# Optimization experiments

Hardware: AMD Instinct MI355X
Metric: run time of the kernel (lower is better)

The kernel has to match this reference:

```python
import jax, jax.numpy as jnp
import numpy as np

T, B, C, H, W, L, K = 8, 8, 64, 96, 96, 2, 3


def _conv(x, w):
    # x: [B,C,H,W], w: [O,I,K,K], SAME padding, stride 1
    return jax.lax.conv_general_dilated(
        x, w, window_strides=(1, 1), padding='SAME',
        dimension_numbers=('NCHW', 'OIHW', 'NCHW'))


def setup_inputs() -> dict:
    key = jax.random.key(0)
    ks = jax.random.split(key, 17)
    wscale = 0.04  # ~ 1/sqrt(64*9) fan-in
    out = {'x': jax.random.normal(ks[0], (T, B, C, H, W), jnp.float32)}
    wnames = ['wxi', 'whi', 'wci', 'wxf', 'whf', 'wcf', 'wxc', 'whc',
              'wxo', 'who', 'wco']
    for i, n in enumerate(wnames):
        out[n] = jax.random.normal(ks[1 + i], (L, C, C, K, K), jnp.float32) * wscale
    bnames = ['b_i', 'b_f', 'b_c', 'b_o']
    for i, n in enumerate(bnames):
        out[n] = jax.random.normal(ks[12 + i], (L, C), jnp.float32) * 0.01
    return out


def reference(x, wxi, whi, wci, wxf, whf, wcf, wxc, whc, wxo, who, wco,
              b_i, b_f, b_c, b_o):
    # x: [T,B,C,H,W]. Peephole Conv-LSTM; note original module's quirk:
    # output gate uses w_hc (with its bias) applied to the NEW cell state.
    hs = cs = None
    for l in range(L):
        Wxi, Whi, Wci = wxi[l], whi[l], wci[l]
        Wxf, Whf, Wcf = wxf[l], whf[l], wcf[l]
        Wxc, Whc = wxc[l], whc[l]
        Wxo, Who, Wco = wxo[l], who[l], wco[l]
        bi = b_i[l][None, :, None, None]
        bf = b_f[l][None, :, None, None]
        bc = b_c[l][None, :, None, None]
        bo = b_o[l][None, :, None, None]

        def step(carry, xt, Wxi=Wxi, Whi=Whi, Wci=Wci, Wxf=Wxf, Whf=Whf,
                 Wcf=Wcf, Wxc=Wxc, Whc=Whc, Wxo=Wxo, Who=Who,
                 bi=bi, bf=bf, bc=bc, bo=bo):
            h, c = carry
            i = jax.nn.sigmoid(_conv(xt, Wxi) + _conv(h, Whi) + bi + _conv(c, Wci))
            f = jax.nn.sigmoid(_conv(xt, Wxf) + _conv(h, Whf) + bf + _conv(c, Wcf))
            c_t = jnp.tanh(_conv(xt, Wxc) + _conv(h, Whc) + bc)
            c_new = c_t * i + c * f
            # faithful to source: w_hc (with its bias) on the new cell state
            o = jax.nn.sigmoid(_conv(xt, Wxo) + _conv(h, Who) + bo
                               + _conv(c_new, Whc) + bc)
            h_new = o * jnp.tanh(c_new)
            return (h_new, c_new), (h_new, c_new)

        h0 = jnp.zeros((x.shape[1], C, H, W), x.dtype)
        c0 = jnp.zeros((x.shape[1], C, H, W), x.dtype)
        _, (hs, cs) = jax.lax.scan(step, (h0, c0), x)
        x = hs  # next layer consumes this layer's hidden sequence
    return hs, cs  # each [T,B,C,H,W]
```

## Files before the change

kernel.cpp:

```cpp
#include <hip/hip_runtime.h>
#include <math.h>

#define TT 8
#define BB 8
#define CC 64
#define HH 96
#define WW 96
#define LL 2
#define HW   (HH * WW)
#define CHW  (CC * HW)
#define BCHW (BB * CHW)
#define TBCHW (TT * BCHW)
#define WSZ  (CC * CC * 9)

typedef _Float16 f16;
typedef __attribute__((ext_vector_type(8))) _Float16 f16x8;
typedef __attribute__((ext_vector_type(4))) _Float16 f16x4;
typedef __attribute__((ext_vector_type(4))) float f32x4;

__device__ __forceinline__ float sigmoidf_(float x) {
    return 1.0f / (1.0f + __expf(-x));
}
__device__ __forceinline__ float tanhf_(float x) {
    float e = __expf(2.f * x);
    return 1.f - 2.f / (e + 1.f);
}


#define SLOT_B   9834496ull
#define PLANE_B  1229312ull
#define SLOT_F   (SLOT_B / 2)
#define GPLANE_F 4718592ull
#define WT_F     36864
#define XHALF_F  18816
#define WHALF_F  18432

struct WPtrs { const float* p[10]; };

__device__ __forceinline__ void gl_lds16(const void* g, void* lds_base) {
    __builtin_amdgcn_global_load_lds(
        (const __attribute__((address_space(1))) unsigned int*)g,
        (__attribute__((address_space(3))) unsigned int*)lds_base, 16, 0, 0);
}

__global__ __launch_bounds__(256) void wprep(WPtrs wsrcs, f16* Wf) {
    const int tap = blockIdx.x, ti = blockIdx.y, l = blockIdx.z;
    const float* src = wsrcs.p[ti] + l * WSZ;
    f16* dst = Wf + (size_t)(l * 10 + ti) * WT_F;
    for (int r = 0; r < 16; ++r) {
        int lin = r * 256 + threadIdx.x;
        int co = lin >> 6, ci = lin & 63;
        float v = src[(co * 64 + ci) * 9 + tap];
        int half = ci >> 5, e = ci & 31, s = e >> 3;
        int p = (s ^ co) & 3;
        dst[((half * 9 + tap) * 64 + co) * 32 + p * 8 + (e & 7)] = (f16)v;
    }
}

__global__ __launch_bounds__(256) void bzero(char* slots) {
    unsigned u = blockIdx.x * 256 + threadIdx.x;
    if (u >= 248320u) return;
    unsigned plane = u / 3104u;
    unsigned r = u % 3104u;
    unsigned i = r >> 3, c = r & 7;
    int y, x;
    if (i < 98)       { y = 0;           x = i; }
    else if (i < 196) { y = 97;          x = i - 98; }
    else if (i < 292) { y = i - 196 + 1; x = 0; }
    else              { y = i - 292 + 1; x = 97; }
    uint4 z = make_uint4(0, 0, 0, 0);
    *(uint4*)(slots + (size_t)plane * PLANE_B + (size_t)(y * 98 + x) * 128 + c * 16) = z;
}

__global__ __launch_bounds__(256) void xprep(const float* __restrict__ x, f16* slots) {
    const int t = blockIdx.y;
    const int b = blockIdx.x / 96, y = blockIdx.x % 96;
    f16* slot = slots + (size_t)t * SLOT_F;
    for (int r = 0; r < 3; ++r) {
        int u = r * 256 + threadIdx.x;
        int px = u >> 3, c = u & 7;
        int half = c >> 2, p = c & 3;
        int sc = (p ^ (px + 1)) & 3;
        int ci0 = half * 32 + sc * 8;
        const float* sp = x + ((((size_t)t * BB + b) * CC + ci0) * HH + y) * WW + px;
        union { f16 h[8]; uint4 q; } pk;
#pragma unroll
        for (int j = 0; j < 8; ++j) pk.h[j] = (f16)sp[(size_t)j * HW];
        f16* dp = slot + ((size_t)b * 9604 + (y + 1) * 98 + (px + 1)) * 64 + half * 32 + p * 8;
        *(uint4*)dp = pk.q;
    }
}

__device__ __forceinline__ void stage_phase(const char* __restrict__ xb_h, int y0,
                                            const char* __restrict__ wsec_h,
                                            int w, int lane, f16* Xs, f16* Wl) {
    const char* xc = xb_h + (size_t)y0 * 12544;
    const int cb = w * 588;
#pragma unroll
    for (int i = 0; i < 9; ++i) {
        const int c = cb + i * 64 + lane;
        gl_lds16(xc + (size_t)(c >> 2) * 128 + (c & 3) * 16,
                 (char*)Xs + (size_t)(cb + i * 64) * 16);
    }
    if (lane < 12) {
        const int c = cb + 576 + lane;
        gl_lds16(xc + (size_t)(c >> 2) * 128 + (c & 3) * 16,
                 (char*)Xs + (size_t)(cb + 576) * 16);
    }
    const int cw = w * 576;
#pragma unroll
    for (int i = 0; i < 9; ++i) {
        gl_lds16(wsec_h + (size_t)(cw + i * 64 + lane) * 16,
                 (char*)Wl + (size_t)(cw + i * 64) * 16);
    }
}

__device__ __forceinline__ void mfma_phase(const f16* Xs, const f16* Wl,
                                           int w, int aBase, int d0, int d1, int d2,
                                           f32x4 acc[4][6]) {
#pragma unroll
    for (int tap = 0; tap < 9; ++tap) {
        const int dy = tap / 3, dx = tap % 3;
        const f16* Ar = &Wl[tap * 2048 + aBase];
        f16x8 a0 = *(const f16x8*)(Ar);
        f16x8 a1 = *(const f16x8*)(Ar + 512);
        f16x8 a2 = *(const f16x8*)(Ar + 1024);
        f16x8 a3 = *(const f16x8*)(Ar + 1536);
        const int doff = (dx == 0) ? d0 : (dx == 1) ? d1 : d2;
        const f16* Br = &Xs[(w + dy) * 3136 + doff];
#pragma unroll
        for (int nt = 0; nt < 6; ++nt) {
            f16x8 bf = *(const f16x8*)(Br + nt * 512);
            acc[0][nt] = __builtin_amdgcn_mfma_f32_16x16x32_f16(a0, bf, acc[0][nt], 0, 0, 0);
            acc[1][nt] = __builtin_amdgcn_mfma_f32_16x16x32_f16(a1, bf, acc[1][nt], 0, 0, 0);
            acc[2][nt] = __builtin_amdgcn_mfma_f32_16x16x32_f16(a2, bf, acc[2][nt], 0, 0, 0);
            acc[3][nt] = __builtin_amdgcn_mfma_f32_16x16x32_f16(a3, bf, acc[3][nt], 0, 0, 0);
        }
    }
}

struct GArgsN {
    const f16* in[3];
    const f16* w[4][3];
    f16* G;
    int nsecA, nsecB;
};

__global__ __launch_bounds__(256, 1) void gates_n(GArgsN A) {
    __shared__ __align__(16) f16 Xs[2 * XHALF_F];
    __shared__ __align__(16) f16 Wl[2 * WHALF_F];
    const int bid = blockIdx.x;
    const int b = bid & 7, rr = bid >> 3, g = rr & 3, y0 = (rr >> 2) * 4;
    const int tid = threadIdx.x, w = tid >> 6, lane = tid & 63;
    const int pxl = lane & 15, kg = lane >> 4;

    const int aBase = pxl * 32 + (((kg ^ pxl) & 3) << 3);
    const int d0 = (pxl + 0) * 32 + (((kg ^ (pxl + 0)) & 3) << 3);
    const int d1 = (pxl + 1) * 32 + (((kg ^ (pxl + 1)) & 3) << 3);
    const int d2 = (pxl + 2) * 32 + (((kg ^ (pxl + 2)) & 3) << 3);

    f32x4 acc[4][6];
#pragma unroll
    for (int mt = 0; mt < 4; ++mt)
#pragma unroll
        for (int nt = 0; nt < 6; ++nt) acc[mt][nt] = (f32x4){0.f, 0.f, 0.f, 0.f};

    const char* xb0 = (const char*)(A.in[0] + (size_t)b * 614656);
    const char* xb1 = (const char*)(A.in[1] + (size_t)b * 614656);
    const char* xb2 = (const char*)(A.in[2] + (size_t)b * 614656);
    const char* wp0 = (const char*)A.w[g][0];
    const char* wp1 = (const char*)A.w[g][1];
    const char* wp2 = (const char*)A.w[g][2];
    const int NP = 2 * ((g < 2) ? A.nsecA : A.nsecB);

    stage_phase(xb0, y0, wp0, w, lane, Xs, Wl);
    __syncthreads();
    for (int p = 0; p < NP; ++p) {
        const int cur = p & 1;
        if (p + 1 < NP) {
            const int s1 = (p + 1) >> 1, h1 = (p + 1) & 1;
            const char* xb_s = (s1 == 0) ? xb0 : (s1 == 1) ? xb1 : xb2;
            const char* wp_s = (s1 == 0) ? wp0 : (s1 == 1) ? wp1 : wp2;
            stage_phase(xb_s + h1 * 64, y0, wp_s + h1 * 36864, w, lane,
                        Xs + (cur ^ 1) * XHALF_F, Wl + (cur ^ 1) * WHALF_F);
        }
        mfma_phase(Xs + cur * XHALF_F, Wl + cur * WHALF_F,
                   w, aBase, d0, d1, d2, acc);
        __syncthreads();
    }

    f16* Gg = A.G + (size_t)g * GPLANE_F + ((size_t)b * 9216 + (y0 + w) * 96) * 64;
#pragma unroll
    for (int mt = 0; mt < 4; ++mt)
#pragma unroll
        for (int nt = 0; nt < 6; ++nt) {
            union { f16 h[4]; uint2 q; } pk;
#pragma unroll
            for (int r = 0; r < 4; ++r) pk.h[r] = (f16)acc[mt][nt][r];
            *(uint2*)(Gg + (size_t)(nt * 16 + pxl) * 64 + mt * 16 + kg * 4) = pk.q;
        }
}

__global__ __launch_bounds__(256) void pointwise_n(const f16* __restrict__ G,
                                                   const f16* __restrict__ cprev,
                                                   const float* __restrict__ bi,
                                                   const float* __restrict__ bf,
                                                   const float* __restrict__ bc,
                                                   f16* __restrict__ cnew,
                                                   float* __restrict__ cs_out) {
    const int b = blockIdx.y;
    const int u = blockIdx.x * 256 + threadIdx.x;
    const int pix = u >> 3, o = u & 7;
    const int ci0 = o * 8;
    const f16x8 gi = *(const f16x8*)(G + ((size_t)b * 9216 + pix) * 64 + ci0);
    const f16x8 gf = *(const f16x8*)(G + GPLANE_F + ((size_t)b * 9216 + pix) * 64 + ci0);
    const f16x8 gc = *(const f16x8*)(G + 2 * GPLANE_F + ((size_t)b * 9216 + pix) * 64 + ci0);
    const int py = pix / 96 + 1, pxp = pix % 96 + 1;
    const size_t pad_off = ((size_t)b * 9604 + py * 98 + pxp) * 64;
    const int half = o >> 2, p = ((o & 3) ^ pxp) & 3;
    const size_t sw_off = pad_off + half * 32 + p * 8;
    f16x8 cp = (f16x8)(_Float16)0.f;
    if (cprev) cp = *(const f16x8*)(cprev + sw_off);
    union { f16 h[8]; uint4 q; } outp;
    float cv[8];
#pragma unroll
    for (int j = 0; j < 8; ++j) {
        float vbi = bi[ci0 + j], vbf = bf[ci0 + j], vbc = bc[ci0 + j];
        float c = tanhf_((float)gc[j] + vbc) * sigmoidf_((float)gi[j] + vbi)
                + (float)cp[j] * sigmoidf_((float)gf[j] + vbf);
        cv[j] = c;
        outp.h[j] = (f16)c;
    }
    *(uint4*)(cnew + sw_off) = outp.q;
    if (cs_out) {
        float* op = cs_out + (size_t)b * CHW + (size_t)ci0 * HW + pix;
#pragma unroll
        for (int j = 0; j < 8; ++j) op[(size_t)j * HW] = cv[j];
    }
}

__global__ __launch_bounds__(256, 1) void out_n(const f16* __restrict__ cnew,
                                                const f16* __restrict__ whc,
                                                const f16* __restrict__ Go,
                                                const float* __restrict__ bo,
                                                const float* __restrict__ bc,
                                                f16* __restrict__ hslot,
                                                float* __restrict__ hs_out) {
    __shared__ __align__(16) f16 Xs[2 * XHALF_F];
    __shared__ __align__(16) f16 Wl[2 * WHALF_F];
    const int bid = blockIdx.x;
    const int b = bid & 7, y0 = (bid >> 3) * 4;
    const int tid = threadIdx.x, w = tid >> 6, lane = tid & 63;
    const int pxl = lane & 15, kg = lane >> 4;

    const int aBase = pxl * 32 + (((kg ^ pxl) & 3) << 3);
    const int d0 = (pxl + 0) * 32 + (((kg ^ (pxl + 0)) & 3) << 3);
    const int d1 = (pxl + 1) * 32 + (((kg ^ (pxl + 1)) & 3) << 3);
    const int d2 = (pxl + 2) * 32 + (((kg ^ (pxl + 2)) & 3) << 3);

    f32x4 acc[4][6];
#pragma unroll
    for (int mt = 0; mt < 4; ++mt)
#pragma unroll
        for (int nt = 0; nt < 6; ++nt) acc[mt][nt] = (f32x4){0.f, 0.f, 0.f, 0.f};

    const char* xb = (const char*)(cnew + (size_t)b * 614656);
    stage_phase(xb, y0, (const char*)whc, w, lane, Xs, Wl);
    __syncthreads();
    for (int p = 0; p < 2; ++p) {
        const int cur = p & 1;
        if (p == 0)
            stage_phase(xb + 64, y0, (const char*)whc + 36864, w, lane,
                        Xs + XHALF_F, Wl + WHALF_F);
        mfma_phase(Xs + cur * XHALF_F, Wl + cur * WHALF_F,
                   w, aBase, d0, d1, d2, acc);
        __syncthreads();
    }

    const int y = y0 + w;
#pragma unroll
    for (int mt = 0; mt < 4; ++mt) {
        const int cob = mt * 16 + kg * 4;
        float vb[4];
#pragma unroll
        for (int r = 0; r < 4; ++r) vb[r] = bo[cob + r] + bc[cob + r];
        const int half = mt >> 1;
        const int sq = (mt * 2 + (kg >> 1)) & 3;
        const int lo4 = (kg & 1) * 4;
#pragma unroll
        for (int nt = 0; nt < 6; ++nt) {
            const int px = nt * 16 + pxl;
            const int pix = y * 96 + px;
            const size_t pad_off = ((size_t)b * 9604 + (y + 1) * 98 + (px + 1)) * 64;
            const int p = (sq ^ (px + 1)) & 3;
            const size_t qoff = pad_off + half * 32 + p * 8 + lo4;
            f16x4 cq = *(const f16x4*)(cnew + qoff);
            f16x4 gq = *(const f16x4*)(Go + ((size_t)b * 9216 + pix) * 64 + cob);
            union { f16 h[4]; uint2 q; } hq;
            float hv[4];
#pragma unroll
            for (int r = 0; r < 4; ++r) {
                float opre = acc[mt][nt][r] + (float)gq[r] + vb[r];
                hv[r] = sigmoidf_(opre) * tanhf_((float)cq[r]);
                hq.h[r] = (f16)hv[r];
            }
            *(uint2*)(hslot + qoff) = hq.q;
            if (hs_out) {
                float* op = hs_out + (size_t)b * CHW + (size_t)cob * HW + pix;
#pragma unroll
                for (int r = 0; r < 4; ++r) op[(size_t)r * HW] = hv[r];
            }
        }
    }
}


#define XROW 3136
#define XSZ  (6 * XROW)
#define WROW 2048
#define WSZL (9 * WROW)

__device__ __forceinline__ void conv_section(
    const float* __restrict__ inb, const float* __restrict__ wp,
    int y0, int tid, f16* Xs, f16* Wl,
    int w, int aBase, int d0, int d1, int d2, f32x4 acc[4][6])
{
    for (int ci0 = 0; ci0 < 64; ci0 += 32) {
        __syncthreads();
        for (int i = tid; i < 9408; i += 256) {
            int x = i % 98; int r = i / 98; int yy = r % 6; int c2 = r / 6;
            int gy = y0 - 1 + yy, gx = x - 1;
            float v0 = 0.f, v1 = 0.f;
            if ((unsigned)gy < 96u && (unsigned)gx < 96u) {
                const float* p = inb + (size_t)(ci0 + 2 * c2) * HW + gy * WW + gx;
                v0 = p[0]; v1 = p[HW];
            }
            union { f16 h[2]; unsigned u; } pk;
            pk.h[0] = (f16)v0; pk.h[1] = (f16)v1;
            int e = 2 * c2;
            int idx = (yy * 98 + x) * 32 + ((((e >> 3) ^ x) & 3) << 3) + (e & 7);
            *(unsigned*)&Xs[idx] = pk.u;
        }
        for (int i = tid; i < 9216; i += 256) {
            int c2 = i & 15; int co = (i >> 4) & 63; int tap = i >> 10;
            const float* p = wp + ((size_t)co * CC + ci0 + 2 * c2) * 9 + tap;
            union { f16 h[2]; unsigned u; } pk;
            pk.h[0] = (f16)p[0]; pk.h[1] = (f16)p[9];
            int e = 2 * c2;
            int idx = tap * WROW + co * 32 + ((((e >> 3) ^ co) & 3) << 3) + (e & 7);
            *(unsigned*)&Wl[idx] = pk.u;
        }
        __syncthreads();
        mfma_phase(Xs, Wl, w, aBase, d0, d1, d2, acc);
    }
}

struct GArgs {
    const float* in[3];
    const float* w[4][3];
    f16* G;
};

__global__ __launch_bounds__(256) void gates_mfma(GArgs A) {
    __shared__ __align__(16) f16 Xs[XSZ];
    __shared__ __align__(16) f16 Wl[WSZL];
    const int g = blockIdx.z, b = blockIdx.y, y0 = blockIdx.x * 4;
    const int tid = threadIdx.x;
    const int w = tid >> 6, lane = tid & 63;
    const int pxl = lane & 15, kg = lane >> 4;
    const int aBase = pxl * 32 + (((kg ^ pxl) & 3) << 3);
    const int d0 = (pxl + 0) * 32 + (((kg ^ (pxl + 0)) & 3) << 3);
    const int d1 = (pxl + 1) * 32 + (((kg ^ (pxl + 1)) & 3) << 3);
    const int d2 = (pxl + 2) * 32 + (((kg ^ (pxl + 2)) & 3) << 3);
    f32x4 acc[4][6];
#pragma unroll
    for (int mt = 0; mt < 4; ++mt)
#pragma unroll
        for (int nt = 0; nt < 6; ++nt) acc[mt][nt] = (f32x4){0.f, 0.f, 0.f, 0.f};
    for (int s = 0; s < 3; ++s) {
        const float* inp = A.in[s];
        const float* wp = A.w[g][s];
        if (!inp || !wp) continue;
        conv_section(inp + (size_t)b * CHW, wp, y0, tid, Xs, Wl, w, aBase, d0, d1, d2, acc);
    }
    f16* Gp = A.G + (size_t)(g * BB + b) * CHW;
    const int y = y0 + w;
#pragma unroll
    for (int mt = 0; mt < 4; ++mt)
#pragma unroll
        for (int r = 0; r < 4; ++r) {
            const int co = mt * 16 + kg * 4 + r;
            f16* rp = Gp + (size_t)co * HW + y * WW + pxl;
#pragma unroll
            for (int nt = 0; nt < 6; ++nt) rp[nt * 16] = (f16)acc[mt][nt][r];
        }
}

__global__ __launch_bounds__(256) void pointwise_c(const f16* __restrict__ G,
                                                   const float* __restrict__ cprev,
                                                   const float* __restrict__ bi,
                                                   const float* __restrict__ bf,
                                                   const float* __restrict__ bc,
                                                   float* __restrict__ cnew) {
    int flat = (blockIdx.x * 256 + threadIdx.x) * 4;
    if (flat >= BCHW) return;
    int co = (flat / HW) & 63;
    f16x4 gi = *(const f16x4*)(G + flat);
    f16x4 gf = *(const f16x4*)(G + (size_t)BCHW + flat);
    f16x4 gc = *(const f16x4*)(G + 2 * (size_t)BCHW + flat);
    float4 cp = make_float4(0.f, 0.f, 0.f, 0.f);
    if (cprev) cp = *(const float4*)(cprev + flat);
    float vbi = bi[co], vbf = bf[co], vbc = bc[co];
    float4 r;
    r.x = tanhf_((float)gc.x + vbc) * sigmoidf_((float)gi.x + vbi) + cp.x * sigmoidf_((float)gf.x + vbf);
    r.y = tanhf_((float)gc.y + vbc) * sigmoidf_((float)gi.y + vbi) + cp.y * sigmoidf_((float)gf.y + vbf);
    r.z = tanhf_((float)gc.z + vbc) * sigmoidf_((float)gi.z + vbi) + cp.z * sigmoidf_((float)gf.z + vbf);
    r.w = tanhf_((float)gc.w + vbc) * sigmoidf_((float)gi.w + vbi) + cp.w * sigmoidf_((float)gf.w + vbf);
    *(float4*)(cnew + flat) = r;
}

__global__ __launch_bounds__(256) void out_mfma(const float* __restrict__ cnew,
                                                const float* __restrict__ wp,
                                                const f16* __restrict__ Go,
                                                const float* __restrict__ bo,
                                                const float* __restrict__ bc,
                                                float* __restrict__ hout) {
    __shared__ __align__(16) f16 Xs[XSZ];
    __shared__ __align__(16) f16 Wl[WSZL];
    const int b = blockIdx.y, y0 = blockIdx.x * 4;
    const int tid = threadIdx.x;
    const int w = tid >> 6, lane = tid & 63;
    const int pxl = lane & 15, kg = lane >> 4;
    const int aBase = pxl * 32 + (((kg ^ pxl) & 3) << 3);
    const int d0 = (pxl + 0) * 32 + (((kg ^ (pxl + 0)) & 3) << 3);
    const int d1 = (pxl + 1) * 32 + (((kg ^ (pxl + 1)) & 3) << 3);
    const int d2 = (pxl + 2) * 32 + (((kg ^ (pxl + 2)) & 3) << 3);
    f32x4 acc[4][6];
#pragma unroll
    for (int mt = 0; mt < 4; ++mt)
#pragma unroll
        for (int nt = 0; nt < 6; ++nt) acc[mt][nt] = (f32x4){0.f, 0.f, 0.f, 0.f};
    const float* cb = cnew + (size_t)b * CHW;
    conv_section(cb, wp, y0, tid, Xs, Wl, w, aBase, d0, d1, d2, acc);
    const f16* Gb = Go + (size_t)b * CHW;
    float* hb = hout + (size_t)b * CHW;
    const int y = y0 + w;
#pragma unroll
    for (int mt = 0; mt < 4; ++mt)
#pragma unroll
        for (int r = 0; r < 4; ++r) {
            const int co = mt * 16 + kg * 4 + r;
            const float vbv = bo[co] + bc[co];
            const size_t off0 = (size_t)co * HW + y * WW + pxl;
#pragma unroll
            for (int nt = 0; nt < 6; ++nt) {
                size_t off = off0 + nt * 16;
                float opre = acc[mt][nt][r] + (float)Gb[off] + vbv;
                hb[off] = sigmoidf_(opre) * tanhf_(cb[off]);
            }
        }
}


extern "C" void kernel_launch(void* const* d_in, const int* in_sizes, int n_in,
                              void* d_out, int out_size, void* d_ws, size_t ws_size,
                              hipStream_t stream) {
    const float* x = (const float*)d_in[0];
    const float* w_[11];
    for (int i = 0; i < 11; ++i) w_[i] = (const float*)d_in[1 + i];
    const float* b_[4];
    for (int i = 0; i < 4; ++i) b_[i] = (const float*)d_in[12 + i];

    float* out = (float*)d_out;
    float* hs = out;
    float* cs = out + TBCHW;

    const size_t G_B = 4ull * GPLANE_F * 2ull;
    const size_t WF_B = 2ull * 10ull * WT_F * 2ull;
    const size_t NEED = 10ull * SLOT_B + G_B + WF_B;

    if (ws_size >= NEED) {
        char* ws = (char*)d_ws;
        f16* slots = (f16*)ws;
        f16* G = (f16*)(ws + 10ull * SLOT_B);
        f16* Wf = (f16*)(ws + 10ull * SLOT_B + G_B);

        WPtrs wps;
        for (int i = 0; i < 10; ++i) wps.p[i] = w_[i];

        wprep<<<dim3(9, 10, 2), 256, 0, stream>>>(wps, Wf);
        bzero<<<dim3(971), 256, 0, stream>>>((char*)slots);
        xprep<<<dim3(96 * BB, TT), 256, 0, stream>>>(x, slots);

        for (int l = 0; l < LL; ++l) {
            const f16* WT[10];
            for (int ti = 0; ti < 10; ++ti) WT[ti] = Wf + (size_t)(l * 10 + ti) * WT_F;
            const float* bi = b_[0] + l * CC;
            const float* bf = b_[1] + l * CC;
            const float* bc = b_[2] + l * CC;
            const float* bo = b_[3] + l * CC;

            for (int t = 0; t < TT; ++t) {
                f16* xt = slots + (size_t)t * SLOT_F;
                f16* hprev = (t == 0) ? nullptr : slots + (size_t)(t - 1) * SLOT_F;
                f16* cprev = (t == 0) ? nullptr
                                      : slots + (size_t)(8 + ((t - 1) & 1)) * SLOT_F;
                f16* cnew = slots + (size_t)(8 + (t & 1)) * SLOT_F;

                GArgsN a;
                if (t == 0) {
                    a.in[0] = xt; a.in[1] = xt; a.in[2] = xt;
                    a.w[0][0] = WT[0]; a.w[0][1] = WT[0]; a.w[0][2] = WT[0];
                    a.w[1][0] = WT[3]; a.w[1][1] = WT[3]; a.w[1][2] = WT[3];
                    a.w[2][0] = WT[6]; a.w[2][1] = WT[6]; a.w[2][2] = WT[6];
                    a.w[3][0] = WT[8]; a.w[3][1] = WT[8]; a.w[3][2] = WT[8];
                    a.nsecA = 1; a.nsecB = 1;
                } else {
                    a.in[0] = xt; a.in[1] = hprev; a.in[2] = cprev;
                    a.w[0][0] = WT[0]; a.w[0][1] = WT[1]; a.w[0][2] = WT[2];
                    a.w[1][0] = WT[3]; a.w[1][1] = WT[4]; a.w[1][2] = WT[5];
                    a.w[2][0] = WT[6]; a.w[2][1] = WT[7]; a.w[2][2] = WT[7];
                    a.w[3][0] = WT[8]; a.w[3][1] = WT[9]; a.w[3][2] = WT[9];
                    a.nsecA = 3; a.nsecB = 2;
                }
                a.G = G;
                gates_n<<<dim3(768), 256, 0, stream>>>(a);
                pointwise_n<<<dim3(288, BB), 256, 0, stream>>>(
                    G, cprev, bi, bf, bc, cnew,
                    (l == 1) ? (cs + (size_t)t * BCHW) : nullptr);
                out_n<<<dim3(192), 256, 0, stream>>>(
                    cnew, WT[7], G + 3 * GPLANE_F, bo, bc,
                    xt,
                    (l == 1) ? (hs + (size_t)t * BCHW) : nullptr);
            }
        }
        return;
    }

    f16* G = (f16*)d_ws;
    float* c0 = (float*)d_ws + 2 * (size_t)BCHW;
    float* c1 = c0 + BCHW;

    for (int l = 0; l < LL; ++l) {
        const float* wxi = w_[0] + l * WSZ;
        const float* whi = w_[1] + l * WSZ;
        const float* wci = w_[2] + l * WSZ;
        const float* wxf = w_[3] + l * WSZ;
        const float* whf = w_[4] + l * WSZ;
        const float* wcf = w_[5] + l * WSZ;
        const float* wxc = w_[6] + l * WSZ;
        const float* whc = w_[7] + l * WSZ;
        const float* wxo = w_[8] + l * WSZ;
        const float* who = w_[9] + l * WSZ;
        const float* bi = b_[0] + l * CC;
        const float* bf = b_[1] + l * CC;
        const float* bc = b_[2] + l * CC;
        const float* bo = b_[3] + l * CC;

        for (int t = 0; t < TT; ++t) {
            const float* xt = (l == 0) ? (x + (size_t)t * BCHW) : (hs + (size_t)t * BCHW);
            const float* hprev = (t == 0) ? nullptr : (hs + (size_t)(t - 1) * BCHW);
            const float* cprev = (t == 0) ? nullptr
                : (l == 0 ? (((t - 1) & 1) ? c1 : c0) : (cs + (size_t)(t - 1) * BCHW));
            float* cnew = (l == 0) ? ((t & 1) ? c1 : c0) : (cs + (size_t)t * BCHW);

            GArgs a;
            a.in[0] = xt; a.in[1] = hprev; a.in[2] = cprev;
            a.w[0][0] = wxi; a.w[0][1] = whi; a.w[0][2] = wci;
            a.w[1][0] = wxf; a.w[1][1] = whf; a.w[1][2] = wcf;
            a.w[2][0] = wxc; a.w[2][1] = whc; a.w[2][2] = nullptr;
            a.w[3][0] = wxo; a.w[3][1] = who; a.w[3][2] = nullptr;
            a.G = G;
            gates_mfma<<<dim3(24, BB, 4), 256, 0, stream>>>(a);
            pointwise_c<<<dim3(BCHW / 1024), 256, 0, stream>>>(G, cprev, bi, bf, bc, cnew);
            out_mfma<<<dim3(24, BB), 256, 0, stream>>>(cnew, whc, G + (size_t)3 * BCHW,
                                                       bo, bc, hs + (size_t)t * BCHW);
        }
    }
}
```

Baseline: 1.716 ms.

## Fuse cell-state pointwise kernel into output-gate conv kernel, computing c_new into LDS

Merges the pointwise cell-update kernel and the output-gate convolution kernel into one. Each block computes c_new for its rows plus a one-row halo directly into shared memory, then runs the w_hc convolution from LDS. This removes a launch and the global round trip of c_new before the conv. The cost is redundant computation of the halo rows, one block per CU, and fewer blocks (192) for the pointwise part. It also switches G loads/stores and the hs/cs float outputs to nontemporal accesses to reduce cache pollution.

```diff
diff --git a/kernel.cpp b/kernel.cpp
--- a/kernel.cpp
+++ b/kernel.cpp
@@ -24,6 +24,16 @@
 __device__ __forceinline__ float tanhf_(float x) {
     float e = __expf(2.f * x);
     return 1.f - 2.f / (e + 1.f);
+}
+
+__device__ __forceinline__ void nt_store_u2(void* p, uint2 v) {
+    __builtin_nontemporal_store(*(unsigned long long*)&v, (unsigned long long*)p);
+}
+__device__ __forceinline__ f16x8 nt_load8(const f16* p) {
+    return __builtin_nontemporal_load((const f16x8*)p);
+}
+__device__ __forceinline__ f16x4 nt_load4(const f16* p) {
+    return __builtin_nontemporal_load((const f16x4*)p);
 }
 
 
@@ -197,55 +207,20 @@
             union { f16 h[4]; uint2 q; } pk;
 #pragma unroll
             for (int r = 0; r < 4; ++r) pk.h[r] = (f16)acc[mt][nt][r];
-            *(uint2*)(Gg + (size_t)(nt * 16 + pxl) * 64 + mt * 16 + kg * 4) = pk.q;
-        }
-}
-
-__global__ __launch_bounds__(256) void pointwise_n(const f16* __restrict__ G,
-                                                   const f16* __restrict__ cprev,
-                                                   const float* __restrict__ bi,
-                                                   const float* __restrict__ bf,
-                                                   const float* __restrict__ bc,
-                                                   f16* __restrict__ cnew,
-                                                   float* __restrict__ cs_out) {
-    const int b = blockIdx.y;
-    const int u = blockIdx.x * 256 + threadIdx.x;
-    const int pix = u >> 3, o = u & 7;
-    const int ci0 = o * 8;
-    const f16x8 gi = *(const f16x8*)(G + ((size_t)b * 9216 + pix) * 64 + ci0);
-    const f16x8 gf = *(const f16x8*)(G + GPLANE_F + ((size_t)b * 9216 + pix) * 64 + ci0);
-    const f16x8 gc = *(const f16x8*)(G + 2 * GPLANE_F + ((size_t)b * 9216 + pix) * 64 + ci0);
-    const int py = pix / 96 + 1, pxp = pix % 96 + 1;
-    const size_t pad_off = ((size_t)b * 9604 + py * 98 + pxp) * 64;
-    const int half = o >> 2, p = ((o & 3) ^ pxp) & 3;
-    const size_t sw_off = pad_off + half * 32 + p * 8;
-    f16x8 cp = (f16x8)(_Float16)0.f;
-    if (cprev) cp = *(const f16x8*)(cprev + sw_off);
-    union { f16 h[8]; uint4 q; } outp;
-    float cv[8];
-#pragma unroll
-    for (int j = 0; j < 8; ++j) {
-        float vbi = bi[ci0 + j], vbf = bf[ci0 + j], vbc = bc[ci0 + j];
-        float c = tanhf_((float)gc[j] + vbc) * sigmoidf_((float)gi[j] + vbi)
-                + (float)cp[j] * sigmoidf_((float)gf[j] + vbf);
-        cv[j] = c;
-        outp.h[j] = (f16)c;
-    }
-    *(uint4*)(cnew + sw_off) = outp.q;
-    if (cs_out) {
-        float* op = cs_out + (size_t)b * CHW + (size_t)ci0 * HW + pix;
-#pragma unroll
-        for (int j = 0; j < 8; ++j) op[(size_t)j * HW] = cv[j];
-    }
-}
-
-__global__ __launch_bounds__(256, 1) void out_n(const f16* __restrict__ cnew,
-                                                const f16* __restrict__ whc,
-                                                const f16* __restrict__ Go,
-                                                const float* __restrict__ bo,
-                                                const float* __restrict__ bc,
-                                                f16* __restrict__ hslot,
-                                                float* __restrict__ hs_out) {
+            nt_store_u2(Gg + (size_t)(nt * 16 + pxl) * 64 + mt * 16 + kg * 4, pk.q);
+        }
+}
+
+__global__ __launch_bounds__(256, 1) void cellout_n(
+    const f16* __restrict__ G,
+    const f16* __restrict__ cprev,
+    const float* __restrict__ bi, const float* __restrict__ bf,
+    const float* __restrict__ bc, const float* __restrict__ bo,
+    const f16* __restrict__ whc,
+    f16* __restrict__ cnew,
+    f16* __restrict__ hslot,
+    float* __restrict__ cs_out,
+    float* __restrict__ hs_out) {
     __shared__ __align__(16) f16 Xs[2 * XHALF_F];
     __shared__ __align__(16) f16 Wl[2 * WHALF_F];
     const int bid = blockIdx.x;
@@ -253,6 +228,79 @@
     const int tid = threadIdx.x, w = tid >> 6, lane = tid & 63;
     const int pxl = lane & 15, kg = lane >> 4;
 
+    {
+        const char* wh = (const char*)whc;
+        const int cw = w * 576;
+#pragma unroll
+        for (int i = 0; i < 9; ++i) {
+            gl_lds16(wh + (size_t)(cw + i * 64 + lane) * 16,
+                     (char*)Wl + (size_t)(cw + i * 64) * 16);
+            gl_lds16(wh + 36864 + (size_t)(cw + i * 64 + lane) * 16,
+                     (char*)(Wl + WHALF_F) + (size_t)(cw + i * 64) * 16);
+        }
+    }
+
+    const int o = tid & 7;
+    const int ci0 = o * 8;
+    const int halfo = o >> 2;
+    float vbi[8], vbf[8], vbc[8];
+#pragma unroll
+    for (int j = 0; j < 8; ++j) { vbi[j] = bi[ci0 + j]; vbf[j] = bf[ci0 + j]; vbc[j] = bc[ci0 + j]; }
+
+    const size_t gb = (size_t)b * 9216;
+    for (int r6 = 0; r6 < 6; ++r6) {
+        const int gy = y0 - 1 + r6;
+        const bool inimg = (unsigned)gy < 96u;
+#pragma unroll
+        for (int j = 0; j < 3; ++j) {
+            const int px = j * 32 + (tid >> 3);
+            const int pxp = px + 1;
+            const int p = ((o & 3) ^ pxp) & 3;
+            union { f16 h[8]; uint4 q; } outp;
+            float cv[8];
+            if (inimg) {
+                const size_t goff = (gb + (size_t)gy * 96 + px) * 64 + ci0;
+                f16x8 gi = nt_load8(G + goff);
+                f16x8 gf = nt_load8(G + GPLANE_F + goff);
+                f16x8 gc = nt_load8(G + 2 * GPLANE_F + goff);
+                f16x8 cp = (f16x8)(_Float16)0.f;
+                if (cprev)
+                    cp = *(const f16x8*)(cprev + ((size_t)b * 9604 + (gy + 1) * 98 + pxp) * 64
+                                          + halfo * 32 + p * 8);
+#pragma unroll
+                for (int jj = 0; jj < 8; ++jj) {
+                    float c = tanhf_((float)gc[jj] + vbc[jj]) * sigmoidf_((float)gi[jj] + vbi[jj])
+                            + (float)cp[jj] * sigmoidf_((float)gf[jj] + vbf[jj]);
+                    cv[jj] = c;
+                    outp.h[jj] = (f16)c;
+                }
+            } else {
+#pragma unroll
+                for (int jj = 0; jj < 8; ++jj) { cv[jj] = 0.f; outp.h[jj] = (f16)0.f; }
+            }
+            *(uint4*)((char*)(Xs + halfo * XHALF_F)
+                      + ((size_t)(r6 * 98 + pxp) * 32 + p * 8) * 2) = outp.q;
+            if (r6 >= 1 && r6 <= 4) {
+                const size_t sw_off = ((size_t)b * 9604 + (gy + 1) * 98 + pxp) * 64
+                                      + halfo * 32 + p * 8;
+                *(uint4*)(cnew + sw_off) = outp.q;
+                if (cs_out) {
+                    float* op = cs_out + (size_t)b * CHW + (size_t)ci0 * HW + gy * 96 + px;
+#pragma unroll
+                    for (int jj = 0; jj < 8; ++jj)
+                        __builtin_nontemporal_store(cv[jj], op + (size_t)jj * HW);
+                }
+            }
+        }
+    }
+    if (tid < 96) {
+        const int e = tid >> 2, q4 = tid & 3;
+        const int hh = e / 12, rem = e % 12, r6 = rem >> 1, col = (rem & 1) * 97;
+        *(uint4*)((char*)(Xs + hh * XHALF_F)
+                  + ((size_t)(r6 * 98 + col) * 32 + q4 * 8) * 2) = make_uint4(0, 0, 0, 0);
+    }
+    __syncthreads();
+
     const int aBase = pxl * 32 + (((kg ^ pxl) & 3) << 3);
     const int d0 = (pxl + 0) * 32 + (((kg ^ (pxl + 0)) & 3) << 3);
     const int d1 = (pxl + 1) * 32 + (((kg ^ (pxl + 1)) & 3) << 3);
@@ -264,18 +312,8 @@
 #pragma unroll
         for (int nt = 0; nt < 6; ++nt) acc[mt][nt] = (f32x4){0.f, 0.f, 0.f, 0.f};
 
-    const char* xb = (const char*)(cnew + (size_t)b * 614656);
-    stage_phase(xb, y0, (const char*)whc, w, lane, Xs, Wl);
-    __syncthreads();
-    for (int p = 0; p < 2; ++p) {
-        const int cur = p & 1;
-        if (p == 0)
-            stage_phase(xb + 64, y0, (const char*)whc + 36864, w, lane,
-                        Xs + XHALF_F, Wl + WHALF_F);
-        mfma_phase(Xs + cur * XHALF_F, Wl + cur * WHALF_F,
-                   w, aBase, d0, d1, d2, acc);
-        __syncthreads();
-    }
+    mfma_phase(Xs, Wl, w, aBase, d0, d1, d2, acc);
+    mfma_phase(Xs + XHALF_F, Wl + WHALF_F, w, aBase, d0, d1, d2, acc);
 
     const int y = y0 + w;
 #pragma unroll
@@ -291,11 +329,13 @@
         for (int nt = 0; nt < 6; ++nt) {
             const int px = nt * 16 + pxl;
             const int pix = y * 96 + px;
-            const size_t pad_off = ((size_t)b * 9604 + (y + 1) * 98 + (px + 1)) * 64;
             const int p = (sq ^ (px + 1)) & 3;
-            const size_t qoff = pad_off + half * 32 + p * 8 + lo4;
-            f16x4 cq = *(const f16x4*)(cnew + qoff);
-            f16x4 gq = *(const f16x4*)(Go + ((size_t)b * 9216 + pix) * 64 + cob);
+            const f16* cl = Xs + half * XHALF_F
+                          + (size_t)((w + 1) * 98 + px + 1) * 32 + p * 8 + lo4;
+            f16x4 cq = *(const f16x4*)cl;
+            f16x4 gq = nt_load4(G + 3 * GPLANE_F + ((size_t)b * 9216 + pix) * 64 + cob);
+            const size_t qoff = ((size_t)b * 9604 + (y + 1) * 98 + (px + 1)) * 64
+                                + half * 32 + p * 8 + lo4;
             union { f16 h[4]; uint2 q; } hq;
             float hv[4];
 #pragma unroll
@@ -308,7 +348,8 @@
             if (hs_out) {
                 float* op = hs_out + (size_t)b * CHW + (size_t)cob * HW + pix;
 #pragma unroll
-                for (int r = 0; r < 4; ++r) op[(size_t)r * HW] = hv[r];
+                for (int r = 0; r < 4; ++r)
+                    __builtin_nontemporal_store(hv[r], op + (size_t)r * HW);
             }
         }
     }
@@ -525,12 +566,10 @@
                 }
                 a.G = G;
                 gates_n<<<dim3(768), 256, 0, stream>>>(a);
-                pointwise_n<<<dim3(288, BB), 256, 0, stream>>>(
-                    G, cprev, bi, bf, bc, cnew,
-                    (l == 1) ? (cs + (size_t)t * BCHW) : nullptr);
-                out_n<<<dim3(192), 256, 0, stream>>>(
-                    cnew, WT[7], G + 3 * GPLANE_F, bo, bc,
+                cellout_n<<<dim3(192), 256, 0, stream>>>(
+                    G, cprev, bi, bf, bc, bo, WT[7], cnew,
                     xt,
+                    (l == 1) ? (cs + (size_t)t * BCHW) : nullptr,
                     (l == 1) ? (hs + (size_t)t * BCHW) : nullptr);
             }
         }
```

Measured after the change: 2.019 ms. +17.7%, slower.

## Compute two gates per block sharing staged input tiles in gates kernel

Applied to the files above, without the earlier changes.

The gates kernel now has each block compute a pair of gates (i/f or c/o) for one 4-row strip, so the staged input tile in LDS is reused across two weight sets instead of being loaded once per gate. Grid size is halved to 384 blocks and each thread holds two accumulator sets. Weight staging is split from input staging and interleaved with the MFMA phases of the other gate. The pointwise kernel switches to a 1D grid with batch in the low bits. The aim is to halve input reads from global memory into LDS, at the cost of doubled accumulator registers and fewer blocks on the device.

```diff
diff --git a/kernel.cpp b/kernel.cpp
--- a/kernel.cpp
+++ b/kernel.cpp
@@ -91,9 +91,8 @@
     }
 }
 
-__device__ __forceinline__ void stage_phase(const char* __restrict__ xb_h, int y0,
-                                            const char* __restrict__ wsec_h,
-                                            int w, int lane, f16* Xs, f16* Wl) {
+__device__ __forceinline__ void stage_x(const char* __restrict__ xb_h, int y0,
+                                        int w, int lane, f16* Xs) {
     const char* xc = xb_h + (size_t)y0 * 12544;
     const int cb = w * 588;
 #pragma unroll
@@ -107,6 +106,9 @@
         gl_lds16(xc + (size_t)(c >> 2) * 128 + (c & 3) * 16,
                  (char*)Xs + (size_t)(cb + 576) * 16);
     }
+}
+__device__ __forceinline__ void stage_w(const char* __restrict__ wsec_h,
+                                        int w, int lane, f16* Wl) {
     const int cw = w * 576;
 #pragma unroll
     for (int i = 0; i < 9; ++i) {
@@ -146,59 +148,93 @@
     int nsecA, nsecB;
 };
 
-__global__ __launch_bounds__(256, 1) void gates_n(GArgsN A) {
+__device__ __forceinline__ const char* wsel(const GArgsN& A, int gate, int sec) {
+    const char* r;
+    if (gate == 0)      r = (const char*)((sec == 0) ? A.w[0][0] : (sec == 1) ? A.w[0][1] : A.w[0][2]);
+    else if (gate == 1) r = (const char*)((sec == 0) ? A.w[1][0] : (sec == 1) ? A.w[1][1] : A.w[1][2]);
+    else if (gate == 2) r = (const char*)((sec == 0) ? A.w[2][0] : A.w[2][1]);
+    else                r = (const char*)((sec == 0) ? A.w[3][0] : A.w[3][1]);
+    return r;
+}
+
+__global__ __launch_bounds__(256, 1) void gates_pair(GArgsN A) {
     __shared__ __align__(16) f16 Xs[2 * XHALF_F];
     __shared__ __align__(16) f16 Wl[2 * WHALF_F];
     const int bid = blockIdx.x;
-    const int b = bid & 7, rr = bid >> 3, g = rr & 3, y0 = (rr >> 2) * 4;
+    const int b = bid & 7, u = bid >> 3;
+    const int gp = u & 1, y0 = (u >> 1) * 4;
     const int tid = threadIdx.x, w = tid >> 6, lane = tid & 63;
     const int pxl = lane & 15, kg = lane >> 4;
+    const int gA = gp * 2, gB = gp * 2 + 1;
+    const int nsec = gp ? A.nsecB : A.nsecA;
+    const int K = 2 * nsec;
 
     const int aBase = pxl * 32 + (((kg ^ pxl) & 3) << 3);
     const int d0 = (pxl + 0) * 32 + (((kg ^ (pxl + 0)) & 3) << 3);
     const int d1 = (pxl + 1) * 32 + (((kg ^ (pxl + 1)) & 3) << 3);
     const int d2 = (pxl + 2) * 32 + (((kg ^ (pxl + 2)) & 3) << 3);
 
-    f32x4 acc[4][6];
+    f32x4 accA[4][6], accB[4][6];
 #pragma unroll
     for (int mt = 0; mt < 4; ++mt)
 #pragma unroll
-        for (int nt = 0; nt < 6; ++nt) acc[mt][nt] = (f32x4){0.f, 0.f, 0.f, 0.f};
+        for (int nt = 0; nt < 6; ++nt) {
+            accA[mt][nt] = (f32x4){0.f, 0.f, 0.f, 0.f};
+            accB[mt][nt] = (f32x4){0.f, 0.f, 0.f, 0.f};
+        }
 
     const char* xb0 = (const char*)(A.in[0] + (size_t)b * 614656);
     const char* xb1 = (const char*)(A.in[1] + (size_t)b * 614656);
     const char* xb2 = (const char*)(A.in[2] + (size_t)b * 614656);
-    const char* wp0 = (const char*)A.w[g][0];
-    const char* wp1 = (const char*)A.w[g][1];
-    const char* wp2 = (const char*)A.w[g][2];
-    const int NP = 2 * ((g < 2) ? A.nsecA : A.nsecB);
-
-    stage_phase(xb0, y0, wp0, w, lane, Xs, Wl);
+
+    stage_x(xb0, y0, w, lane, Xs);
+    stage_w(wsel(A, gA, 0), w, lane, Wl);
     __syncthreads();
-    for (int p = 0; p < NP; ++p) {
-        const int cur = p & 1;
-        if (p + 1 < NP) {
-            const int s1 = (p + 1) >> 1, h1 = (p + 1) & 1;
-            const char* xb_s = (s1 == 0) ? xb0 : (s1 == 1) ? xb1 : xb2;
-            const char* wp_s = (s1 == 0) ? wp0 : (s1 == 1) ? wp1 : wp2;
-            stage_phase(xb_s + h1 * 64, y0, wp_s + h1 * 36864, w, lane,
-                        Xs + (cur ^ 1) * XHALF_F, Wl + (cur ^ 1) * WHALF_F);
-        }
-        mfma_phase(Xs + cur * XHALF_F, Wl + cur * WHALF_F,
-                   w, aBase, d0, d1, d2, acc);
+
+    for (int k = 0; k < K; ++k) {
+        const int cur = k & 1;
+        const int s = k >> 1, h = k & 1;
+        if (k + 1 < K) {
+            const int s1 = (k + 1) >> 1, h1 = (k + 1) & 1;
+            const char* xbn = (s1 == 0) ? xb0 : (s1 == 1) ? xb1 : xb2;
+            stage_x(xbn + h1 * 64, y0, w, lane, Xs + ((k + 1) & 1) * XHALF_F);
+        }
+        stage_w(wsel(A, gB, s) + h * 36864, w, lane, Wl + WHALF_F);
+        mfma_phase(Xs + cur * XHALF_F, Wl, w, aBase, d0, d1, d2, accA);
         __syncthreads();
-    }
-
-    f16* Gg = A.G + (size_t)g * GPLANE_F + ((size_t)b * 9216 + (y0 + w) * 96) * 64;
-#pragma unroll
-    for (int mt = 0; mt < 4; ++mt)
-#pragma unroll
-        for (int nt = 0; nt < 6; ++nt) {
-            union { f16 h[4]; uint2 q; } pk;
-#pragma unroll
-            for (int r = 0; r < 4; ++r) pk.h[r] = (f16)acc[mt][nt][r];
-            *(uint2*)(Gg + (size_t)(nt * 16 + pxl) * 64 + mt * 16 + kg * 4) = pk.q;
-        }
+        if (k + 1 < K) {
+            const int s1 = (k + 1) >> 1, h1 = (k + 1) & 1;
+            stage_w(wsel(A, gA, s1) + h1 * 36864, w, lane, Wl);
+        }
+        mfma_phase(Xs + cur * XHALF_F, Wl + WHALF_F, w, aBase, d0, d1, d2, accB);
+        __syncthreads();
+    }
+
+    const size_t rowoff = ((size_t)b * 9216 + (y0 + w) * 96) * 64;
+    {
+        f16* Gg = A.G + (size_t)gA * GPLANE_F + rowoff;
+#pragma unroll
+        for (int mt = 0; mt < 4; ++mt)
+#pragma unroll
+            for (int nt = 0; nt < 6; ++nt) {
+                union { f16 h[4]; uint2 q; } pk;
+#pragma unroll
+                for (int r = 0; r < 4; ++r) pk.h[r] = (f16)accA[mt][nt][r];
+                *(uint2*)(Gg + (size_t)(nt * 16 + pxl) * 64 + mt * 16 + kg * 4) = pk.q;
+            }
+    }
+    {
+        f16* Gg = A.G + (size_t)gB * GPLANE_F + rowoff;
+#pragma unroll
+        for (int mt = 0; mt < 4; ++mt)
+#pragma unroll
+            for (int nt = 0; nt < 6; ++nt) {
+                union { f16 h[4]; uint2 q; } pk;
+#pragma unroll
+                for (int r = 0; r < 4; ++r) pk.h[r] = (f16)accB[mt][nt][r];
+                *(uint2*)(Gg + (size_t)(nt * 16 + pxl) * 64 + mt * 16 + kg * 4) = pk.q;
+            }
+    }
 }
 
 __global__ __launch_bounds__(256) void pointwise_n(const f16* __restrict__ G,
@@ -208,13 +244,15 @@
                                                    const float* __restrict__ bc,
                                                    f16* __restrict__ cnew,
                                                    float* __restrict__ cs_out) {
-    const int b = blockIdx.y;
-    const int u = blockIdx.x * 256 + threadIdx.x;
+    const int bid = blockIdx.x;
+    const int b = bid & 7;
+    const int u = (bid >> 3) * 256 + threadIdx.x;
     const int pix = u >> 3, o = u & 7;
     const int ci0 = o * 8;
-    const f16x8 gi = *(const f16x8*)(G + ((size_t)b * 9216 + pix) * 64 + ci0);
-    const f16x8 gf = *(const f16x8*)(G + GPLANE_F + ((size_t)b * 9216 + pix) * 64 + ci0);
-    const f16x8 gc = *(const f16x8*)(G + 2 * GPLANE_F + ((size_t)b * 9216 + pix) * 64 + ci0);
+    const size_t goff = ((size_t)b * 9216 + pix) * 64 + ci0;
+    const f16x8 gi = *(const f16x8*)(G + goff);
+    const f16x8 gf = *(const f16x8*)(G + GPLANE_F + goff);
+    const f16x8 gc = *(const f16x8*)(G + 2 * GPLANE_F + goff);
     const int py = pix / 96 + 1, pxp = pix % 96 + 1;
     const size_t pad_off = ((size_t)b * 9604 + py * 98 + pxp) * 64;
     const int half = o >> 2, p = ((o & 3) ^ pxp) & 3;
@@ -265,13 +303,15 @@
         for (int nt = 0; nt < 6; ++nt) acc[mt][nt] = (f32x4){0.f, 0.f, 0.f, 0.f};
 
     const char* xb = (const char*)(cnew + (size_t)b * 614656);
-    stage_phase(xb, y0, (const char*)whc, w, lane, Xs, Wl);
+    stage_x(xb, y0, w, lane, Xs);
+    stage_w((const char*)whc, w, lane, Wl);
     __syncthreads();
     for (int p = 0; p < 2; ++p) {
         const int cur = p & 1;
-        if (p == 0)
-            stage_phase(xb + 64, y0, (const char*)whc + 36864, w, lane,
-                        Xs + XHALF_F, Wl + WHALF_F);
+        if (p == 0) {
+            stage_x(xb + 64, y0, w, lane, Xs + XHALF_F);
+            stage_w((const char*)whc + 36864, w, lane, Wl + WHALF_F);
+        }
         mfma_phase(Xs + cur * XHALF_F, Wl + cur * WHALF_F,
                    w, aBase, d0, d1, d2, acc);
         __syncthreads();
@@ -524,8 +564,8 @@
                     a.nsecA = 3; a.nsecB = 2;
                 }
                 a.G = G;
-                gates_n<<<dim3(768), 256, 0, stream>>>(a);
-                pointwise_n<<<dim3(288, BB), 256, 0, stream>>>(
+                gates_pair<<<dim3(384), 256, 0, stream>>>(a);
+                pointwise_n<<<dim3(2304), 256, 0, stream>>>(
                     G, cprev, bi, bf, bc, cnew,
                     (l == 1) ? (cs + (size_t)t * BCHW) : nullptr);
                 out_n<<<dim3(192), 256, 0, stream>>>(
```

Measured after the change: 2.104 ms. +22.6%, slower.
